# Performance work log

Hardware: AMD Instinct MI355X
Metric: run time of the kernel (lower is better)

Reference implementation:

```python
import jax, jax.numpy as jnp
import numpy as np

B, S, E, H = 2, 2048, 1024, 16
D = E // H  # head size = 64


def setup_inputs() -> dict:
    key = jax.random.key(0)
    ks = jax.random.split(key, 13)
    scale = 1.0 / np.sqrt(E)
    inp = {
        "q": jax.random.normal(ks[0], (B, S, E), jnp.float32),
        "k": jax.random.normal(ks[1], (B, S, E), jnp.float32),
        "v": jax.random.normal(ks[2], (B, S, E), jnp.float32),
        "mask": jax.random.randint(ks[3], (B, 1, S, S), 0, 2, jnp.int32),
        "Wq": jax.random.normal(ks[4], (E, E), jnp.float32) * scale,
        "bq": jnp.zeros((E,), jnp.float32),
        "Wk": jax.random.normal(ks[5], (E, E), jnp.float32) * scale,
        "bk": jnp.zeros((E,), jnp.float32),
        "Wv": jax.random.normal(ks[6], (E, E), jnp.float32) * scale,
        "bv": jnp.zeros((E,), jnp.float32),
        "Wo": jax.random.normal(ks[7], (E, E), jnp.float32) * scale,
        "bo": jnp.zeros((E,), jnp.float32),
    }
    return inp


def reference(q, k, v, mask, Wq, bq, Wk, bk, Wv, bv, Wo, bo):
    # Linear projections (torch Linear: x @ W.T + b)
    qh = (q @ Wq.T + bq).reshape(B, S, H, D).transpose(0, 2, 1, 3)  # [B,H,S,D]
    kh = (k @ Wk.T + bk).reshape(B, S, H, D).transpose(0, 2, 1, 3)
    vh = (v @ Wv.T + bv).reshape(B, S, H, D).transpose(0, 2, 1, 3)

    scores = jnp.einsum("bhqd,bhkd->bhqk", qh, kh) / jnp.sqrt(jnp.float32(D))
    scores = jnp.where(mask == 0, jnp.float32(-1e10), scores)
    attn = jax.nn.softmax(scores, axis=-1)  # [B,H,S,S]
    ctx = jnp.einsum("bhqk,bhkd->bhqd", attn, vh)  # dropout p=0.0 -> identity

    out = ctx.transpose(0, 2, 1, 3).reshape(B, S, E)
    return out @ Wo.T + bo
```

## Files before the change

### kernel.cpp

```cpp
#include <hip/hip_runtime.h>

typedef unsigned short ushort_t;
typedef __attribute__((ext_vector_type(8))) short short8;
typedef __attribute__((ext_vector_type(4))) float f32x4;
typedef __attribute__((ext_vector_type(4))) unsigned short ushort4_t;
typedef __attribute__((ext_vector_type(2))) unsigned int uint2_t;
typedef __attribute__((ext_vector_type(4))) unsigned int uint4_t;

#define BB 2
#define SS 2048
#define EE 1024
#define HH 16
#define DD 64
#define MM (BB*SS)

#define QB_OFF  0u
#define KB_OFF  4194304u
#define VB_OFF  8388608u
#define WQ_OFF  12582912u
#define WK_OFF  13631488u
#define WV_OFF  14680064u
#define WO_OFF  15728640u
#define QH_OFF  16777216u
#define KH_OFF  20971520u
#define VT_OFF  25165824u
#define CTX_OFF QB_OFF
#define MB_OFF  29360128u

__device__ __forceinline__ ushort_t f2bf(float x) {
    unsigned u = __builtin_bit_cast(unsigned, x);
    u += 0x7FFFu + ((u >> 16) & 1u);
    return (ushort_t)(u >> 16);
}

__device__ __forceinline__ unsigned pk_bf16(float a, float b) {
    unsigned ua = __builtin_bit_cast(unsigned, a);
    unsigned ub = __builtin_bit_cast(unsigned, b);
    ua += 0x7FFFu + ((ua >> 16) & 1u);
    ub += 0x7FFFu + ((ub >> 16) & 1u);
    return __builtin_amdgcn_perm(ub, ua, 0x07060302u);
}

__device__ __forceinline__ void load_lds16(const void* g, void* l) {
    __builtin_amdgcn_global_load_lds((const __attribute__((address_space(1))) void*)g,
                                     (__attribute__((address_space(3))) void*)l, 16, 0, 0);
}

__global__ __launch_bounds__(256) void prep_kernel(
    const float* __restrict__ q, const float* __restrict__ k, const float* __restrict__ v,
    const int* __restrict__ mask,
    const float* __restrict__ Wq, const float* __restrict__ Wk,
    const float* __restrict__ Wv, const float* __restrict__ Wo,
    ushort_t* __restrict__ wsb, unsigned* __restrict__ maskbits)
{
    int g = blockIdx.x;
    if (g < 16384) {
        int idx = g * 256 + threadIdx.x;
        const float* src; ushort_t* dst; int rel;
        if      (idx < 1048576) { src = q;  dst = wsb + QB_OFF; rel = idx; }
        else if (idx < 2097152) { src = k;  dst = wsb + KB_OFF; rel = idx - 1048576; }
        else if (idx < 3145728) { src = v;  dst = wsb + VB_OFF; rel = idx - 2097152; }
        else if (idx < 3407872) { src = Wq; dst = wsb + WQ_OFF; rel = idx - 3145728; }
        else if (idx < 3670016) { src = Wk; dst = wsb + WK_OFF; rel = idx - 3407872; }
        else if (idx < 3932160) { src = Wv; dst = wsb + WV_OFF; rel = idx - 3670016; }
        else                    { src = Wo; dst = wsb + WO_OFF; rel = idx - 3932160; }
        f32x4 val = ((const f32x4*)src)[rel];
        ushort4_t o;
        o.x = f2bf(val.x); o.y = f2bf(val.y); o.z = f2bf(val.z); o.w = f2bf(val.w);
        ((ushort4_t*)dst)[rel] = o;
    } else {
        int t = (g - 16384) * 256 + threadIdx.x;
        int b   = t >> 17;
        int rem = t & 131071;
        int w   = rem >> 11;
        int sk  = rem & 2047;
        unsigned bits = 0;
        const int* mp = mask + ((size_t)b * SS + (size_t)w * 32) * SS + sk;
        #pragma unroll
        for (int jj = 0; jj < 32; ++jj)
            bits |= (mp[(size_t)jj * SS] != 0 ? 1u : 0u) << jj;
        maskbits[((size_t)b * SS + sk) * 64 + w] = bits;
    }
}

__device__ __forceinline__ void gemm_mainloop(
    const ushort_t* __restrict__ A, const ushort_t* __restrict__ Bm,
    int m0, int n0, f32x4 acc[4][4], ushort_t* As, ushort_t* Bs)
{
    const int tid  = threadIdx.x;
    const int wave = tid >> 6, lane = tid & 63;
    const int r16  = lane >> 2;
    const int c8   = (lane & 3) * 8;
    const int lane15 = lane & 15, quad = lane >> 4;
    const int wm = wave >> 1, wn = wave & 1;

    #pragma unroll 1
    for (int kt = 0; kt < 32; ++kt) {
        const int k0 = kt * 32;
        __syncthreads();
        const ushort_t* ga = A  + (size_t)(m0 + wave * 32 + r16) * 1024 + k0 + c8;
        load_lds16(ga,             As + wave * 1024);
        load_lds16(ga + 16 * 1024, As + wave * 1024 + 512);
        const ushort_t* gb = Bm + (size_t)(n0 + wave * 32 + r16) * 1024 + k0 + c8;
        load_lds16(gb,             Bs + wave * 1024);
        load_lds16(gb + 16 * 1024, Bs + wave * 1024 + 512);
        __syncthreads();

        short8 a[4], bf[4];
        #pragma unroll
        for (int i = 0; i < 4; ++i)
            a[i] = *(const short8*)&As[(wm * 64 + i * 16 + lane15) * 32 + quad * 8];
        #pragma unroll
        for (int j = 0; j < 4; ++j)
            bf[j] = *(const short8*)&Bs[(wn * 64 + j * 16 + lane15) * 32 + quad * 8];
        #pragma unroll
        for (int i = 0; i < 4; ++i)
            #pragma unroll
            for (int j = 0; j < 4; ++j)
                acc[i][j] = __builtin_amdgcn_mfma_f32_16x16x32_bf16(a[i], bf[j], acc[i][j], 0, 0, 0);
    }
}

__global__ __launch_bounds__(256) void gemm_qkv(
    ushort_t* __restrict__ wsb,
    const float* __restrict__ bq, const float* __restrict__ bk, const float* __restrict__ bv)
{
    __shared__ ushort_t As[128 * 32], Bs[128 * 32];
    const int z = blockIdx.z;
    const ushort_t* A;
    const ushort_t* Bm;
    if      (z == 0) { A = wsb + QB_OFF; Bm = wsb + WQ_OFF; }
    else if (z == 1) { A = wsb + KB_OFF; Bm = wsb + WK_OFF; }
    else             { A = wsb + WV_OFF; Bm = wsb + VB_OFF; }
    const float* bias  = (z == 0) ? bq : (z == 1) ? bk : bv;
    ushort_t* dst      = wsb + (z == 0 ? QH_OFF : z == 1 ? KH_OFF : VT_OFF);
    const int m0 = (z < 2) ? blockIdx.y * 128 : blockIdx.x * 128;
    const int n0 = (z < 2) ? blockIdx.x * 128 : blockIdx.y * 128;

    f32x4 acc[4][4];
    #pragma unroll
    for (int i = 0; i < 4; ++i)
        #pragma unroll
        for (int j = 0; j < 4; ++j) acc[i][j] = (f32x4){0.f, 0.f, 0.f, 0.f};

    gemm_mainloop(A, Bm, m0, n0, acc, As, Bs);

    const int tid = threadIdx.x, wave = tid >> 6, lane = tid & 63;
    const int lane15 = lane & 15, quad = lane >> 4;
    const int wm = wave >> 1, wn = wave & 1;
    const float scale = (z == 0) ? 0.180336880111f : 1.0f;

    if (z < 2) {
        #pragma unroll
        for (int i = 0; i < 4; ++i) {
            #pragma unroll
            for (int j = 0; j < 4; ++j) {
                int col = n0 + wn * 64 + j * 16 + lane15;
                float bv_ = bias[col];
                int hh = col >> 6, d = col & 63;
                #pragma unroll
                for (int r = 0; r < 4; ++r) {
                    int row = m0 + wm * 64 + i * 16 + quad * 4 + r;
                    int bb = row >> 11, s = row & 2047;
                    float val = (acc[i][j][r] + bv_) * scale;
                    dst[(((size_t)bb * HH + hh) * SS + s) * DD + d] = f2bf(val);
                }
            }
        }
    } else {
        #pragma unroll
        for (int i = 0; i < 4; ++i) {
            #pragma unroll
            for (int r = 0; r < 4; ++r) {
                int row = m0 + wm * 64 + i * 16 + quad * 4 + r;
                float bv_ = bias[row];
                int hh = row >> 6, d = row & 63;
                #pragma unroll
                for (int j = 0; j < 4; ++j) {
                    int col = n0 + wn * 64 + j * 16 + lane15;
                    int bb = col >> 11, s = col & 2047;
                    int kk = s & 127;
                    int sp = ((kk >> 6) << 6) | ((kk & 15) << 2) | ((kk >> 4) & 3);
                    dst[(((size_t)bb * HH + hh) * DD + d) * SS + (s & ~127) + sp]
                        = f2bf(acc[i][j][r] + bv_);
                }
            }
        }
    }
}

__global__ __launch_bounds__(256, 2) void attn_kernel(
    const ushort_t* __restrict__ wsb, const unsigned* __restrict__ maskbits,
    ushort_t* __restrict__ ctx)
{
    __shared__ ushort_t Ks[128 * 64];
    __shared__ ushort_t Vts[64 * 128];
    __shared__ ushort_t Ps[128 * 64];

    const int tid  = threadIdx.x;
    const int wave = tid >> 6, lane = tid & 63;
    const int lane15 = lane & 15, quad = lane >> 4;
    const int sw7 = lane15 & 7;
    const int bh = blockIdx.y;
    const int b  = bh >> 4, h = bh & 15;
    const int q0 = blockIdx.x * 128;

    const ushort_t* Qh  = wsb + QH_OFF;
    const ushort_t* Kh  = wsb + KH_OFF;
    const ushort_t* VhT = wsb + VT_OFF;

    short8 qfrag[2][2];
    #pragma unroll
    for (int i = 0; i < 2; ++i)
        #pragma unroll
        for (int ks = 0; ks < 2; ++ks)
            qfrag[i][ks] = *(const short8*)(Qh +
                ((size_t)bh * SS + q0 + wave * 32 + i * 16 + lane15) * DD + ks * 32 + quad * 8);

    short8 ones_frag;
    {
        short onev = (lane15 == 0) ? (short)0x3F80 : (short)0;
        #pragma unroll
        for (int e = 0; e < 8; ++e) ones_frag[e] = onev;
    }

    const f32x4 zero4 = (f32x4){0.f, 0.f, 0.f, 0.f};
    f32x4 s_acc[2][8];
    f32x4 o_acc[2][4];
    f32x4 osum[2];
    #pragma unroll
    for (int i = 0; i < 2; ++i) {
        #pragma unroll
        for (int jd = 0; jd < 4; ++jd) o_acc[i][jd] = zero4;
        osum[i] = zero4;
    }

    #pragma unroll 1
    for (int kt = 0; kt < 16; ++kt) {
        const int k0 = kt * 128;
        __syncthreads();

        const ushort_t* Kbase = Kh + ((size_t)bh * SS + k0) * DD;
        #pragma unroll
        for (int cc = 0; cc < 4; ++cc) {
            int n = (wave * 4 + cc) * 64 + lane;
            int row = n >> 3;
            int c = (n & 7) ^ (row & 7);
            load_lds16(Kbase + row * 64 + c * 8, Ks + (wave * 4 + cc) * 512);
        }
        const ushort_t* Vbase = VhT + ((size_t)bh * DD) * SS + k0;
        #pragma unroll
        for (int cc = 0; cc < 4; ++cc) {
            int n = (wave * 4 + cc) * 64 + lane;
            int d = n >> 4;
            int c = (n & 15) ^ (d & 7);
            load_lds16(Vbase + (size_t)d * SS + c * 8, Vts + (wave * 4 + cc) * 512);
        }

        unsigned mw[8];
        {
            const int qw = (q0 >> 5) + wave;
            #pragma unroll
            for (int j = 0; j < 8; ++j) {
                int sk = k0 + j * 16 + lane15;
                mw[j] = maskbits[((size_t)b * SS + sk) * 64 + qw];
            }
        }
        __syncthreads();

        #pragma unroll
        for (int j = 0; j < 8; ++j) {
            short8 bf = *(const short8*)&Ks[(j * 16 + lane15) * 64 + ((quad ^ sw7) << 3)];
            s_acc[0][j] = __builtin_amdgcn_mfma_f32_16x16x32_bf16(qfrag[0][0], bf, zero4, 0, 0, 0);
            s_acc[1][j] = __builtin_amdgcn_mfma_f32_16x16x32_bf16(qfrag[1][0], bf, zero4, 0, 0, 0);
        }
        #pragma unroll
        for (int j = 0; j < 8; ++j) {
            short8 bf = *(const short8*)&Ks[(j * 16 + lane15) * 64 + (((4 + quad) ^ sw7) << 3)];
            s_acc[0][j] = __builtin_amdgcn_mfma_f32_16x16x32_bf16(qfrag[0][1], bf, s_acc[0][j], 0, 0, 0);
            s_acc[1][j] = __builtin_amdgcn_mfma_f32_16x16x32_bf16(qfrag[1][1], bf, s_acc[1][j], 0, 0, 0);
        }

        #pragma unroll
        for (int ph = 0; ph < 2; ++ph) {
            #pragma unroll
            for (int i = 0; i < 2; ++i) {
                #pragma unroll
                for (int r = 0; r < 4; ++r) {
                    const int bit = i * 16 + quad * 4 + r;
                    float p[4];
                    #pragma unroll
                    for (int jj = 0; jj < 4; ++jj) {
                        float e = __builtin_amdgcn_exp2f(s_acc[i][ph * 4 + jj][r]);
                        p[jj] = ((mw[ph * 4 + jj] >> bit) & 1u) ? e : 0.f;
                    }
                    uint2_t pk;
                    pk.x = pk_bf16(p[0], p[1]);
                    pk.y = pk_bf16(p[2], p[3]);
                    const int row = wave * 32 + i * 16 + quad * 4 + r;
                    *(uint2_t*)&Ps[row * 64 +
                        ((((lane15 >> 1) ^ (row & 7)) << 3) + ((lane15 & 1) << 2))] = pk;
                }
            }

            #pragma unroll
            for (int kb = 0; kb < 2; ++kb) {
                short8 ap[2];
                #pragma unroll
                for (int i = 0; i < 2; ++i)
                    ap[i] = *(const short8*)&Ps[(wave * 32 + i * 16 + lane15) * 64 +
                                                (((kb * 4 + quad) ^ sw7) << 3)];
                #pragma unroll
                for (int jd = 0; jd < 4; ++jd) {
                    short8 bv_ = *(const short8*)&Vts[(jd * 16 + lane15) * 128 +
                                                      (((ph * 8 + kb * 4 + quad) ^ sw7) << 3)];
                    o_acc[0][jd] = __builtin_amdgcn_mfma_f32_16x16x32_bf16(ap[0], bv_, o_acc[0][jd], 0, 0, 0);
                    o_acc[1][jd] = __builtin_amdgcn_mfma_f32_16x16x32_bf16(ap[1], bv_, o_acc[1][jd], 0, 0, 0);
                }
                osum[0] = __builtin_amdgcn_mfma_f32_16x16x32_bf16(ap[0], ones_frag, osum[0], 0, 0, 0);
                osum[1] = __builtin_amdgcn_mfma_f32_16x16x32_bf16(ap[1], ones_frag, osum[1], 0, 0, 0);
            }
        }
    }

    #pragma unroll
    for (int i = 0; i < 2; ++i) {
        #pragma unroll
        for (int r = 0; r < 4; ++r) {
            float l = __shfl(osum[i][r], lane & 48);
            float inv = 1.0f / l;
            int row = q0 + wave * 32 + i * 16 + quad * 4 + r;
            #pragma unroll
            for (int jd = 0; jd < 4; ++jd) {
                int col = h * DD + jd * 16 + lane15;
                ctx[((size_t)b * SS + row) * EE + col] = f2bf(o_acc[i][jd][r] * inv);
            }
        }
    }
}

__global__ __launch_bounds__(256) void gemm_out(
    const ushort_t* __restrict__ wsb, const float* __restrict__ bo, float* __restrict__ out)
{
    __shared__ ushort_t As[64 * 32];
    __shared__ ushort_t Bs[128 * 32];
    const ushort_t* A  = wsb + CTX_OFF;
    const ushort_t* Bm = wsb + WO_OFF;
    const int m0 = blockIdx.y * 64, n0 = blockIdx.x * 128;

    const int tid = threadIdx.x, wave = tid >> 6, lane = tid & 63;
    const int lane15 = lane & 15, quad = lane >> 4;

    f32x4 acc[8];
    #pragma unroll
    for (int j = 0; j < 8; ++j) acc[j] = (f32x4){0.f, 0.f, 0.f, 0.f};

    #pragma unroll 1
    for (int kt = 0; kt < 32; ++kt) {
        const int k0 = kt * 32;
        __syncthreads();
        {
            int n = wave * 64 + lane;
            load_lds16(A + (size_t)(m0 + (n >> 2)) * 1024 + k0 + (n & 3) * 8,
                       As + wave * 512);
        }
        #pragma unroll
        for (int m = 0; m < 2; ++m) {
            int n = m * 256 + wave * 64 + lane;
            load_lds16(Bm + (size_t)(n0 + (n >> 2)) * 1024 + k0 + (n & 3) * 8,
                       Bs + (m * 256 + wave * 64) * 8);
        }
        __syncthreads();

        short8 a = *(const short8*)&As[(wave * 16 + lane15) * 32 + quad * 8];
        #pragma unroll
        for (int j = 0; j < 8; ++j) {
            short8 bf = *(const short8*)&Bs[(j * 16 + lane15) * 32 + quad * 8];
            acc[j] = __builtin_amdgcn_mfma_f32_16x16x32_bf16(a, bf, acc[j], 0, 0, 0);
        }
    }

    #pragma unroll
    for (int j = 0; j < 8; ++j) {
        int col = n0 + j * 16 + lane15;
        float bv_ = bo[col];
        #pragma unroll
        for (int r = 0; r < 4; ++r) {
            int row = m0 + wave * 16 + quad * 4 + r;
            out[(size_t)row * EE + col] = acc[j][r] + bv_;
        }
    }
}

extern "C" void kernel_launch(void* const* d_in, const int* in_sizes, int n_in,
                              void* d_out, int out_size, void* d_ws, size_t ws_size,
                              hipStream_t stream) {
    const float* q    = (const float*)d_in[0];
    const float* k    = (const float*)d_in[1];
    const float* v    = (const float*)d_in[2];
    const int*   mask = (const int*)  d_in[3];
    const float* Wq   = (const float*)d_in[4];
    const float* bq   = (const float*)d_in[5];
    const float* Wk   = (const float*)d_in[6];
    const float* bk   = (const float*)d_in[7];
    const float* Wv   = (const float*)d_in[8];
    const float* bv   = (const float*)d_in[9];
    const float* Wo   = (const float*)d_in[10];
    const float* bo   = (const float*)d_in[11];

    ushort_t* wsb = (ushort_t*)d_ws;
    unsigned* maskbits = (unsigned*)(wsb + MB_OFF);

    prep_kernel<<<17408, 256, 0, stream>>>(q, k, v, mask, Wq, Wk, Wv, Wo, wsb, maskbits);
    gemm_qkv<<<dim3(8, 32, 3), 256, 0, stream>>>(wsb, bq, bk, bv);
    attn_kernel<<<dim3(16, 32), 256, 0, stream>>>(wsb, maskbits, wsb + CTX_OFF);
    gemm_out<<<dim3(8, 64), 256, 0, stream>>>(wsb, bo, (float*)d_out);
}
```

Measured before the change: 289.3 us.

## Split attention block across 8 waves with 16 query rows each

New measurement: 296.6 us. 2.5% more time.

```diff
diff --git a/kernel.cpp b/kernel.cpp
--- a/kernel.cpp
+++ b/kernel.cpp
@@ -189,7 +189,7 @@
     }
 }
 
-__global__ __launch_bounds__(256, 2) void attn_kernel(
+__global__ __launch_bounds__(512, 4) void attn_kernel(
     const ushort_t* __restrict__ wsb, const unsigned* __restrict__ maskbits,
     ushort_t* __restrict__ ctx)
 {
@@ -209,13 +209,11 @@
     const ushort_t* Kh  = wsb + KH_OFF;
     const ushort_t* VhT = wsb + VT_OFF;
 
-    short8 qfrag[2][2];
-    #pragma unroll
-    for (int i = 0; i < 2; ++i)
-        #pragma unroll
-        for (int ks = 0; ks < 2; ++ks)
-            qfrag[i][ks] = *(const short8*)(Qh +
-                ((size_t)bh * SS + q0 + wave * 32 + i * 16 + lane15) * DD + ks * 32 + quad * 8);
+    short8 qfrag[2];
+    #pragma unroll
+    for (int ks = 0; ks < 2; ++ks)
+        qfrag[ks] = *(const short8*)(Qh +
+            ((size_t)bh * SS + q0 + wave * 16 + lane15) * DD + ks * 32 + quad * 8);
 
     short8 ones_frag;
     {
@@ -225,15 +223,11 @@
     }
 
     const f32x4 zero4 = (f32x4){0.f, 0.f, 0.f, 0.f};
-    f32x4 s_acc[2][8];
-    f32x4 o_acc[2][4];
-    f32x4 osum[2];
-    #pragma unroll
-    for (int i = 0; i < 2; ++i) {
-        #pragma unroll
-        for (int jd = 0; jd < 4; ++jd) o_acc[i][jd] = zero4;
-        osum[i] = zero4;
-    }
+    f32x4 s_acc[8];
+    f32x4 o_acc[4];
+    f32x4 osum = zero4;
+    #pragma unroll
+    for (int jd = 0; jd < 4; ++jd) o_acc[jd] = zero4;
 
     #pragma unroll 1
     for (int kt = 0; kt < 16; ++kt) {
@@ -242,24 +236,24 @@
 
         const ushort_t* Kbase = Kh + ((size_t)bh * SS + k0) * DD;
         #pragma unroll
-        for (int cc = 0; cc < 4; ++cc) {
-            int n = (wave * 4 + cc) * 64 + lane;
+        for (int cc = 0; cc < 2; ++cc) {
+            int n = (wave * 2 + cc) * 64 + lane;
             int row = n >> 3;
             int c = (n & 7) ^ (row & 7);
-            load_lds16(Kbase + row * 64 + c * 8, Ks + (wave * 4 + cc) * 512);
+            load_lds16(Kbase + row * 64 + c * 8, Ks + (wave * 2 + cc) * 512);
         }
         const ushort_t* Vbase = VhT + ((size_t)bh * DD) * SS + k0;
         #pragma unroll
-        for (int cc = 0; cc < 4; ++cc) {
-            int n = (wave * 4 + cc) * 64 + lane;
+        for (int cc = 0; cc < 2; ++cc) {
+            int n = (wave * 2 + cc) * 64 + lane;
             int d = n >> 4;
             int c = (n & 15) ^ (d & 7);
-            load_lds16(Vbase + (size_t)d * SS + c * 8, Vts + (wave * 4 + cc) * 512);
+            load_lds16(Vbase + (size_t)d * SS + c * 8, Vts + (wave * 2 + cc) * 512);
         }
 
         unsigned mw[8];
         {
-            const int qw = (q0 >> 5) + wave;
+            const int qw = (q0 >> 5) + (wave >> 1);
             #pragma unroll
             for (int j = 0; j < 8; ++j) {
                 int sk = k0 + j * 16 + lane15;
@@ -271,70 +265,57 @@
         #pragma unroll
         for (int j = 0; j < 8; ++j) {
             short8 bf = *(const short8*)&Ks[(j * 16 + lane15) * 64 + ((quad ^ sw7) << 3)];
-            s_acc[0][j] = __builtin_amdgcn_mfma_f32_16x16x32_bf16(qfrag[0][0], bf, zero4, 0, 0, 0);
-            s_acc[1][j] = __builtin_amdgcn_mfma_f32_16x16x32_bf16(qfrag[1][0], bf, zero4, 0, 0, 0);
+            s_acc[j] = __builtin_amdgcn_mfma_f32_16x16x32_bf16(qfrag[0], bf, zero4, 0, 0, 0);
         }
         #pragma unroll
         for (int j = 0; j < 8; ++j) {
             short8 bf = *(const short8*)&Ks[(j * 16 + lane15) * 64 + (((4 + quad) ^ sw7) << 3)];
-            s_acc[0][j] = __builtin_amdgcn_mfma_f32_16x16x32_bf16(qfrag[0][1], bf, s_acc[0][j], 0, 0, 0);
-            s_acc[1][j] = __builtin_amdgcn_mfma_f32_16x16x32_bf16(qfrag[1][1], bf, s_acc[1][j], 0, 0, 0);
+            s_acc[j] = __builtin_amdgcn_mfma_f32_16x16x32_bf16(qfrag[1], bf, s_acc[j], 0, 0, 0);
         }
 
         #pragma unroll
         for (int ph = 0; ph < 2; ++ph) {
             #pragma unroll
-            for (int i = 0; i < 2; ++i) {
+            for (int r = 0; r < 4; ++r) {
+                const int bit = (wave & 1) * 16 + quad * 4 + r;
+                float p[4];
                 #pragma unroll
-                for (int r = 0; r < 4; ++r) {
-                    const int bit = i * 16 + quad * 4 + r;
-                    float p[4];
-                    #pragma unroll
-                    for (int jj = 0; jj < 4; ++jj) {
-                        float e = __builtin_amdgcn_exp2f(s_acc[i][ph * 4 + jj][r]);
-                        p[jj] = ((mw[ph * 4 + jj] >> bit) & 1u) ? e : 0.f;
-                    }
-                    uint2_t pk;
-                    pk.x = pk_bf16(p[0], p[1]);
-                    pk.y = pk_bf16(p[2], p[3]);
-                    const int row = wave * 32 + i * 16 + quad * 4 + r;
-                    *(uint2_t*)&Ps[row * 64 +
-                        ((((lane15 >> 1) ^ (row & 7)) << 3) + ((lane15 & 1) << 2))] = pk;
+                for (int jj = 0; jj < 4; ++jj) {
+                    float e = __builtin_amdgcn_exp2f(s_acc[ph * 4 + jj][r]);
+                    p[jj] = ((mw[ph * 4 + jj] >> bit) & 1u) ? e : 0.f;
                 }
+                uint2_t pk;
+                pk.x = pk_bf16(p[0], p[1]);
+                pk.y = pk_bf16(p[2], p[3]);
+                const int row = wave * 16 + quad * 4 + r;
+                *(uint2_t*)&Ps[row * 64 +
+                    ((((lane15 >> 1) ^ (row & 7)) << 3) + ((lane15 & 1) << 2))] = pk;
             }
 
             #pragma unroll
             for (int kb = 0; kb < 2; ++kb) {
-                short8 ap[2];
-                #pragma unroll
-                for (int i = 0; i < 2; ++i)
-                    ap[i] = *(const short8*)&Ps[(wave * 32 + i * 16 + lane15) * 64 +
+                short8 ap = *(const short8*)&Ps[(wave * 16 + lane15) * 64 +
                                                 (((kb * 4 + quad) ^ sw7) << 3)];
                 #pragma unroll
                 for (int jd = 0; jd < 4; ++jd) {
                     short8 bv_ = *(const short8*)&Vts[(jd * 16 + lane15) * 128 +
                                                       (((ph * 8 + kb * 4 + quad) ^ sw7) << 3)];
-                    o_acc[0][jd] = __builtin_amdgcn_mfma_f32_16x16x32_bf16(ap[0], bv_, o_acc[0][jd], 0, 0, 0);
-                    o_acc[1][jd] = __builtin_amdgcn_mfma_f32_16x16x32_bf16(ap[1], bv_, o_acc[1][jd], 0, 0, 0);
+                    o_acc[jd] = __builtin_amdgcn_mfma_f32_16x16x32_bf16(ap, bv_, o_acc[jd], 0, 0, 0);
                 }
-                osum[0] = __builtin_amdgcn_mfma_f32_16x16x32_bf16(ap[0], ones_frag, osum[0], 0, 0, 0);
-                osum[1] = __builtin_amdgcn_mfma_f32_16x16x32_bf16(ap[1], ones_frag, osum[1], 0, 0, 0);
-            }
-        }
-    }
-
-    #pragma unroll
-    for (int i = 0; i < 2; ++i) {
-        #pragma unroll
-        for (int r = 0; r < 4; ++r) {
-            float l = __shfl(osum[i][r], lane & 48);
-            float inv = 1.0f / l;
-            int row = q0 + wave * 32 + i * 16 + quad * 4 + r;
-            #pragma unroll
-            for (int jd = 0; jd < 4; ++jd) {
-                int col = h * DD + jd * 16 + lane15;
-                ctx[((size_t)b * SS + row) * EE + col] = f2bf(o_acc[i][jd][r] * inv);
-            }
+                osum = __builtin_amdgcn_mfma_f32_16x16x32_bf16(ap, ones_frag, osum, 0, 0, 0);
+            }
+        }
+    }
+
+    #pragma unroll
+    for (int r = 0; r < 4; ++r) {
+        float l = __shfl(osum[r], lane & 48);
+        float inv = 1.0f / l;
+        int row = q0 + wave * 16 + quad * 4 + r;
+        #pragma unroll
+        for (int jd = 0; jd < 4; ++jd) {
+            int col = h * DD + jd * 16 + lane15;
+            ctx[((size_t)b * SS + row) * EE + col] = f2bf(o_acc[jd][r] * inv);
         }
     }
 }
@@ -413,6 +394,6 @@
 
     prep_kernel<<<17408, 256, 0, stream>>>(q, k, v, mask, Wq, Wk, Wv, Wo, wsb, maskbits);
     gemm_qkv<<<dim3(8, 32, 3), 256, 0, stream>>>(wsb, bq, bk, bv);
-    attn_kernel<<<dim3(16, 32), 256, 0, stream>>>(wsb, maskbits, wsb + CTX_OFF);
+    attn_kernel<<<dim3(16, 32), 512, 0, stream>>>(wsb, maskbits, wsb + CTX_OFF);
     gemm_out<<<dim3(8, 64), 256, 0, stream>>>(wsb, bo, (float*)d_out);
 }
```

## Double-buffer K/V tiles and mask bits in attention, swizzle blocks across XCDs

Applied to the files above, without the earlier changes.

New measurement: 294.7 us. About the same (+1.9%).

```diff
diff --git a/kernel.cpp b/kernel.cpp
--- a/kernel.cpp
+++ b/kernel.cpp
@@ -193,21 +193,25 @@
     const ushort_t* __restrict__ wsb, const unsigned* __restrict__ maskbits,
     ushort_t* __restrict__ ctx)
 {
-    __shared__ ushort_t Ks[128 * 64];
-    __shared__ ushort_t Vts[64 * 128];
+    __shared__ ushort_t Ks[2][128 * 64];
+    __shared__ ushort_t Vts[2][64 * 128];
     __shared__ ushort_t Ps[128 * 64];
 
     const int tid  = threadIdx.x;
     const int wave = tid >> 6, lane = tid & 63;
     const int lane15 = lane & 15, quad = lane >> 4;
     const int sw7 = lane15 & 7;
-    const int bh = blockIdx.y;
-    const int b  = bh >> 4, h = bh & 15;
-    const int q0 = blockIdx.x * 128;
+    const int bid = blockIdx.x;
+    const int swz = (bid & 7) * 64 + (bid >> 3);
+    const int bh  = swz >> 4;
+    const int q0  = (swz & 15) * 128;
+    const int b   = bh >> 4, h = bh & 15;
 
     const ushort_t* Qh  = wsb + QH_OFF;
     const ushort_t* Kh  = wsb + KH_OFF;
     const ushort_t* VhT = wsb + VT_OFF;
+    const ushort_t* Kbase0 = Kh + (size_t)bh * SS * DD;
+    const ushort_t* Vbase0 = VhT + (size_t)bh * DD * SS;
 
     short8 qfrag[2][2];
     #pragma unroll
@@ -235,48 +239,70 @@
         osum[i] = zero4;
     }
 
+    const int kn   = (wave * 4) * 64 + lane;
+    const int qw   = (q0 >> 5) + wave;
+
+    unsigned mwc[8], mwn[8];
+    {
+        #pragma unroll
+        for (int cc = 0; cc < 4; ++cc) {
+            int n = kn + cc * 64;
+            int row = n >> 3;
+            int c = (n & 7) ^ (row & 7);
+            load_lds16(Kbase0 + row * 64 + c * 8, &Ks[0][(wave * 4 + cc) * 512]);
+        }
+        #pragma unroll
+        for (int cc = 0; cc < 4; ++cc) {
+            int n = kn + cc * 64;
+            int d = n >> 4;
+            int c = (n & 15) ^ (d & 7);
+            load_lds16(Vbase0 + (size_t)d * SS + c * 8, &Vts[0][(wave * 4 + cc) * 512]);
+        }
+        #pragma unroll
+        for (int j = 0; j < 8; ++j)
+            mwc[j] = maskbits[((size_t)b * SS + j * 16 + lane15) * 64 + qw];
+    }
+
     #pragma unroll 1
     for (int kt = 0; kt < 16; ++kt) {
-        const int k0 = kt * 128;
+        const int cur = kt & 1;
         __syncthreads();
 
-        const ushort_t* Kbase = Kh + ((size_t)bh * SS + k0) * DD;
-        #pragma unroll
-        for (int cc = 0; cc < 4; ++cc) {
-            int n = (wave * 4 + cc) * 64 + lane;
-            int row = n >> 3;
-            int c = (n & 7) ^ (row & 7);
-            load_lds16(Kbase + row * 64 + c * 8, Ks + (wave * 4 + cc) * 512);
-        }
-        const ushort_t* Vbase = VhT + ((size_t)bh * DD) * SS + k0;
-        #pragma unroll
-        for (int cc = 0; cc < 4; ++cc) {
-            int n = (wave * 4 + cc) * 64 + lane;
-            int d = n >> 4;
-            int c = (n & 15) ^ (d & 7);
-            load_lds16(Vbase + (size_t)d * SS + c * 8, Vts + (wave * 4 + cc) * 512);
-        }
-
-        unsigned mw[8];
-        {
-            const int qw = (q0 >> 5) + wave;
-            #pragma unroll
-            for (int j = 0; j < 8; ++j) {
-                int sk = k0 + j * 16 + lane15;
-                mw[j] = maskbits[((size_t)b * SS + sk) * 64 + qw];
-            }
-        }
-        __syncthreads();
+        if (kt < 15) {
+            const int k0n = (kt + 1) * 128;
+            const ushort_t* Kb = Kbase0 + (size_t)k0n * DD;
+            #pragma unroll
+            for (int cc = 0; cc < 4; ++cc) {
+                int n = kn + cc * 64;
+                int row = n >> 3;
+                int c = (n & 7) ^ (row & 7);
+                load_lds16(Kb + row * 64 + c * 8, &Ks[cur ^ 1][(wave * 4 + cc) * 512]);
+            }
+            const ushort_t* Vb = Vbase0 + k0n;
+            #pragma unroll
+            for (int cc = 0; cc < 4; ++cc) {
+                int n = kn + cc * 64;
+                int d = n >> 4;
+                int c = (n & 15) ^ (d & 7);
+                load_lds16(Vb + (size_t)d * SS + c * 8, &Vts[cur ^ 1][(wave * 4 + cc) * 512]);
+            }
+            #pragma unroll
+            for (int j = 0; j < 8; ++j)
+                mwn[j] = maskbits[((size_t)b * SS + k0n + j * 16 + lane15) * 64 + qw];
+        }
+
+        const ushort_t* ksr = &Ks[cur][0];
+        const ushort_t* vsr = &Vts[cur][0];
 
         #pragma unroll
         for (int j = 0; j < 8; ++j) {
-            short8 bf = *(const short8*)&Ks[(j * 16 + lane15) * 64 + ((quad ^ sw7) << 3)];
+            short8 bf = *(const short8*)&ksr[(j * 16 + lane15) * 64 + ((quad ^ sw7) << 3)];
             s_acc[0][j] = __builtin_amdgcn_mfma_f32_16x16x32_bf16(qfrag[0][0], bf, zero4, 0, 0, 0);
             s_acc[1][j] = __builtin_amdgcn_mfma_f32_16x16x32_bf16(qfrag[1][0], bf, zero4, 0, 0, 0);
         }
         #pragma unroll
         for (int j = 0; j < 8; ++j) {
-            short8 bf = *(const short8*)&Ks[(j * 16 + lane15) * 64 + (((4 + quad) ^ sw7) << 3)];
+            short8 bf = *(const short8*)&ksr[(j * 16 + lane15) * 64 + (((4 + quad) ^ sw7) << 3)];
             s_acc[0][j] = __builtin_amdgcn_mfma_f32_16x16x32_bf16(qfrag[0][1], bf, s_acc[0][j], 0, 0, 0);
             s_acc[1][j] = __builtin_amdgcn_mfma_f32_16x16x32_bf16(qfrag[1][1], bf, s_acc[1][j], 0, 0, 0);
         }
@@ -292,7 +318,7 @@
                     #pragma unroll
                     for (int jj = 0; jj < 4; ++jj) {
                         float e = __builtin_amdgcn_exp2f(s_acc[i][ph * 4 + jj][r]);
-                        p[jj] = ((mw[ph * 4 + jj] >> bit) & 1u) ? e : 0.f;
+                        p[jj] = ((mwc[ph * 4 + jj] >> bit) & 1u) ? e : 0.f;
                     }
                     uint2_t pk;
                     pk.x = pk_bf16(p[0], p[1]);
@@ -312,7 +338,7 @@
                                                 (((kb * 4 + quad) ^ sw7) << 3)];
                 #pragma unroll
                 for (int jd = 0; jd < 4; ++jd) {
-                    short8 bv_ = *(const short8*)&Vts[(jd * 16 + lane15) * 128 +
+                    short8 bv_ = *(const short8*)&vsr[(jd * 16 + lane15) * 128 +
                                                       (((ph * 8 + kb * 4 + quad) ^ sw7) << 3)];
                     o_acc[0][jd] = __builtin_amdgcn_mfma_f32_16x16x32_bf16(ap[0], bv_, o_acc[0][jd], 0, 0, 0);
                     o_acc[1][jd] = __builtin_amdgcn_mfma_f32_16x16x32_bf16(ap[1], bv_, o_acc[1][jd], 0, 0, 0);
@@ -321,6 +347,9 @@
                 osum[1] = __builtin_amdgcn_mfma_f32_16x16x32_bf16(ap[1], ones_frag, osum[1], 0, 0, 0);
             }
         }
+
+        #pragma unroll
+        for (int j = 0; j < 8; ++j) mwc[j] = mwn[j];
     }
 
     #pragma unroll
@@ -413,6 +442,6 @@
 
     prep_kernel<<<17408, 256, 0, stream>>>(q, k, v, mask, Wq, Wk, Wv, Wo, wsb, maskbits);
     gemm_qkv<<<dim3(8, 32, 3), 256, 0, stream>>>(wsb, bq, bk, bv);
-    attn_kernel<<<dim3(16, 32), 256, 0, stream>>>(wsb, maskbits, wsb + CTX_OFF);
+    attn_kernel<<<512, 256, 0, stream>>>(wsb, maskbits, wsb + CTX_OFF);
     gemm_out<<<dim3(8, 64), 256, 0, stream>>>(wsb, bo, (float*)d_out);
 }
```
